# Kernel tuning notes

Hardware: AMD Instinct MI355X
Metric: run time of the kernel (lower is better)

The kernel has to match this reference:

```python
import jax, jax.numpy as jnp
import numpy as np

B, M, T, H = 256, 80, 1000, 128


def setup_inputs() -> dict:
    key = jax.random.key(0)
    k1, k2, k3, k4, k5 = jax.random.split(key, 5)
    s = 1.0 / np.sqrt(H)
    x = jax.random.normal(k1, (B, M, T), dtype=jnp.float32)
    W_ih = jax.random.uniform(k2, (3 * H, M), dtype=jnp.float32, minval=-s, maxval=s)
    W_hh = jax.random.uniform(k3, (3 * H, H), dtype=jnp.float32, minval=-s, maxval=s)
    b_ih = jax.random.uniform(k4, (3 * H,), dtype=jnp.float32, minval=-s, maxval=s)
    b_hh = jax.random.uniform(k5, (3 * H,), dtype=jnp.float32, minval=-s, maxval=s)
    return {"x": x, "W_ih": W_ih, "W_hh": W_hh, "b_ih": b_ih, "b_hh": b_hh}


def reference(x, W_ih, W_hh, b_ih, b_hh):
    # x: (B, n_mels, T) -> (B, T, n_mels)
    xt = jnp.swapaxes(x, 1, 2)
    # Precompute input-side gate projections for all timesteps: (B, T, 3H)
    gx_all = jnp.einsum('btm,gm->btg', xt, W_ih) + b_ih
    gx_seq = jnp.swapaxes(gx_all, 0, 1)  # (T, B, 3H)

    def step(h, gx):
        gh = h @ W_hh.T + b_hh  # (B, 3H)
        xr, xz, xn = jnp.split(gx, 3, axis=-1)
        hr, hz, hn = jnp.split(gh, 3, axis=-1)
        r = jax.nn.sigmoid(xr + hr)
        z = jax.nn.sigmoid(xz + hz)
        n = jnp.tanh(xn + r * hn)
        h_new = (1.0 - z) * n + z * h
        return h_new, None

    h0 = jnp.zeros((x.shape[0], H), dtype=x.dtype)
    hT, _ = jax.lax.scan(step, h0, gx_seq)
    return hT  # (B, H) == hidden[-1]
```

## Files before the change

kernel.cpp:

```cpp
#include <hip/hip_runtime.h>
#include <stdint.h>

#define B_   256
#define M_   80
#define T_   1000
#define H_   128
#define TILE 32
#define NT_  32
#define XPAD 104
#define GXS  520

typedef _Float16 half8  __attribute__((ext_vector_type(8)));
typedef _Float16 half4v __attribute__((ext_vector_type(4)));
typedef float    f32x4  __attribute__((ext_vector_type(4)));

#define LOG2E 1.44269504f
#define MFMA(A, Bf, C) __builtin_amdgcn_mfma_f32_16x16x32_f16((A), (Bf), (C), 0, 0, 0)

__device__ __forceinline__ float fast_sigmoid(float v) {
    return __builtin_amdgcn_rcpf(1.0f + __builtin_amdgcn_exp2f(-LOG2E * v));
}
__device__ __forceinline__ float fast_tanh(float v) {
    return fmaf(-2.0f, __builtin_amdgcn_rcpf(1.0f + __builtin_amdgcn_exp2f(2.0f * LOG2E * v)), 1.0f);
}

__global__ __launch_bounds__(512, 2) void gru_tile(
    const float* __restrict__ x,
    const float* __restrict__ W_ih,
    const float* __restrict__ W_hh,
    const float* __restrict__ b_ih,
    const float* __restrict__ b_hh,
    float* __restrict__ out)
{
    const int b   = blockIdx.x;
    const int tid = threadIdx.x;
    const int l   = tid & 63;
    const int w   = tid >> 6;
    const int jn  = l & 15;
    const int kq  = l >> 4;
    const int hid = 16 * w + jn;

    __shared__ __align__(16) _Float16 gxt[TILE][GXS];
    __shared__ __align__(16) _Float16 xt16[2][TILE][XPAD];
    __shared__ __align__(16) _Float16 h16[2][H_];

    half8 wr[4], wz[4], wn[4];
#pragma unroll
    for (int f = 0; f < 4; ++f)
#pragma unroll
        for (int j = 0; j < 8; ++j) {
            const int k = 32 * f + 8 * kq + j;
            wr[f][j] = (_Float16)W_hh[(hid)          * H_ + k];
            wz[f][j] = (_Float16)W_hh[(H_ + hid)     * H_ + k];
            wn[f][j] = (_Float16)W_hh[(2 * H_ + hid) * H_ + k];
        }
#pragma unroll
    for (int f = 0; f < 4; ++f) {
        asm volatile("" : "+v"(wr[f]));
        asm volatile("" : "+v"(wz[f]));
        asm volatile("" : "+v"(wn[f]));
    }

    half8 wih[3][3];
    float biasA[3];
#pragma unroll
    for (int i = 0; i < 3; ++i) {
        const int g = 16 * (3 * w + i) + jn;
        biasA[i] = b_ih[g] + (g < 2 * H_ ? b_hh[g] : 0.0f);
        const float* wp = W_ih + g * M_;
#pragma unroll
        for (int f = 0; f < 3; ++f)
#pragma unroll
            for (int j = 0; j < 8; ++j) {
                const int k = 32 * f + 8 * kq + j;
                wih[i][f][j] = (k < M_) ? (_Float16)wp[k] : (_Float16)0.0f;
            }
    }
#pragma unroll
    for (int i = 0; i < 3; ++i) {
        asm volatile("" : "+v"(wih[i][0]));
        asm volatile("" : "+v"(wih[i][1]));
        asm volatile("" : "+v"(wih[i][2]));
    }
    asm volatile("" : "+v"(biasA[0]), "+v"(biasA[1]), "+v"(biasA[2]));

    const float bN = b_hh[2 * H_ + hid];
    const f32x4 zero4 = { 0.f, 0.f, 0.f, 0.f };
    const f32x4 bN4   = { bN, bN, bN, bN };
    const float* xb = x + (size_t)b * M_ * T_;

    for (int i = tid; i < 2 * TILE * XPAD; i += 512) ((short*)xt16)[i] = 0;
    if (tid < H_) h16[0][tid] = (_Float16)0.0f;
    __syncthreads();
    {
        const int tq = tid & 7, m0 = tid >> 3;
        float4 v0 = *(const float4*)&xb[(size_t)m0 * T_ + 4 * tq];
#pragma unroll
        for (int e = 0; e < 4; ++e) xt16[0][4 * tq + e][m0] = (_Float16)v0[e];
        if (tid < 128) {
            float4 v1 = *(const float4*)&xb[(size_t)(64 + m0) * T_ + 4 * tq];
#pragma unroll
            for (int e = 0; e < 4; ++e) xt16[0][4 * tq + e][64 + m0] = (_Float16)v1[e];
        }
    }
    __syncthreads();

    float h_r = 0.0f;

#define GRU_STEP(RB, WB, CA, PA_, TN)                                         \
    {                                                                         \
        const int ko = 8 * kq;                                                \
        const half8 a0 = *(const half8*)&h16[RB][ko];                         \
        const half8 a2 = *(const half8*)&h16[RB][64 + ko];                    \
        const half8 a1 = *(const half8*)&h16[RB][32 + ko];                    \
        const half8 a3 = *(const half8*)&h16[RB][96 + ko];                    \
        PA_ = *(const half4v*)&gxt[TN][hid * 4];                              \
        const float gr = (float)CA[0], gz = (float)CA[1], gn = (float)CA[2];  \
        f32x4 Ra = MFMA(a0, wr[0], zero4);                                    \
        f32x4 Na = MFMA(a0, wn[0], bN4);                                      \
        f32x4 Rb = MFMA(a2, wr[2], zero4);                                    \
        f32x4 Nb = MFMA(a2, wn[2], zero4);                                    \
        Ra = MFMA(a1, wr[1], Ra);                                             \
        Na = MFMA(a1, wn[1], Na);                                             \
        Rb = MFMA(a3, wr[3], Rb);                                             \
        Nb = MFMA(a3, wn[3], Nb);                                             \
        f32x4 Zc = MFMA(a0, wz[0], zero4);                                    \
        Zc = MFMA(a1, wz[1], Zc);                                             \
        Zc = MFMA(a2, wz[2], Zc);                                             \
        Zc = MFMA(a3, wz[3], Zc);                                             \
        const float r  = fast_sigmoid(Ra[0] + Rb[0] + gr);                    \
        const float nv = fast_tanh(fmaf(r, Na[0] + Nb[0], gn));               \
        const float z  = fast_sigmoid(Zc[0] + gz);                            \
        h_r = fmaf(z, h_r - nv, nv);                                          \
        if (l < 16) h16[WB][hid] = (_Float16)h_r;                             \
    }

    for (int tb = 0; tb < NT_; ++tb) {
        const int t1 = TILE * (tb + 1);
        const int tq = tid & 7, m0 = tid >> 3;
        float4 xv0, xv1;
        const bool doPref = (t1 < T_);
        if (doPref) {
            const int tc0 = t1 + 4 * tq;
            const int tc  = (tc0 <= T_ - 4) ? tc0 : (T_ - 4);
            xv0 = *(const float4*)&xb[(size_t)m0 * T_ + tc];
            if (tid < 128) xv1 = *(const float4*)&xb[(size_t)(64 + m0) * T_ + tc];
        }
        const int cbuf = tb & 1, nbuf = cbuf ^ 1;
#pragma unroll
        for (int mt = 0; mt < 2; ++mt) {
            half8 af[3];
#pragma unroll
            for (int f = 0; f < 3; ++f)
                af[f] = *(const half8*)&xt16[cbuf][16 * mt + jn][32 * f + 8 * kq];
#pragma unroll
            for (int i = 0; i < 3; ++i) {
                f32x4 acc = { biasA[i], biasA[i], biasA[i], biasA[i] };
                acc = MFMA(af[0], wih[i][0], acc);
                acc = MFMA(af[1], wih[i][1], acc);
                acc = MFMA(af[2], wih[i][2], acc);
                const int g    = 16 * (3 * w + i) + jn;
                const int cc   = (g & 127) * 4 + (g >> 7);
                const int trow = 16 * mt + 4 * kq;
#pragma unroll
                for (int r2 = 0; r2 < 4; ++r2)
                    gxt[trow + r2][cc] = (_Float16)acc[r2];
            }
        }
        if (doPref) {
#pragma unroll
            for (int e = 0; e < 4; ++e) xt16[nbuf][4 * tq + e][m0] = (_Float16)xv0[e];
            if (tid < 128) {
#pragma unroll
                for (int e = 0; e < 4; ++e) xt16[nbuf][4 * tq + e][64 + m0] = (_Float16)xv1[e];
            }
        }
        __syncthreads();

        const int rem    = T_ - TILE * tb;
        const int nsteps = (rem < TILE) ? rem : TILE;

        half4v gC = *(const half4v*)&gxt[0][hid * 4];
        half4v gP;

        for (int tt = 0; tt < nsteps; tt += 2) {
            GRU_STEP(0, 1, gC, gP, tt + 1);
            __syncthreads();
            const int tn2 = (tt + 2 < nsteps) ? (tt + 2) : 0;
            GRU_STEP(1, 0, gP, gC, tn2);
            __syncthreads();
        }
    }

    if (l < 16) out[(size_t)b * H_ + hid] = h_r;
}

extern "C" void kernel_launch(void* const* d_in, const int* in_sizes, int n_in,
                              void* d_out, int out_size, void* d_ws, size_t ws_size,
                              hipStream_t stream) {
    const float* x    = (const float*)d_in[0];
    const float* W_ih = (const float*)d_in[1];
    const float* W_hh = (const float*)d_in[2];
    const float* b_ih = (const float*)d_in[3];
    const float* b_hh = (const float*)d_in[4];
    float* out = (float*)d_out;

    gru_tile<<<dim3(B_), dim3(512), 0, stream>>>(x, W_ih, W_hh, b_ih, b_hh, out);
}
```

Measured before the change: 459.5 us.

## Software-pipeline input projection across recurrent steps with double-buffered gate tile

The input-gate projection for the next time tile is now computed one MFMA triple at a time between recurrent steps of the current tile, instead of in a separate phase before each tile's recurrence. The gate buffer becomes double-buffered with an XOR-swizzled layout to reduce LDS bank conflicts, and the x prefetch is moved two tiles ahead. s_setprio is raised around the recurrent MFMA chain. The aim is to hide the per-tile projection and sync latency inside the serial recurrence, at the cost of more LDS and more complex indexing.

Measured after the change: 513.9 us. 1.12x slower.

```diff
diff --git a/kernel.cpp b/kernel.cpp
--- a/kernel.cpp
+++ b/kernel.cpp
@@ -22,6 +22,10 @@
 }
 __device__ __forceinline__ float fast_tanh(float v) {
     return fmaf(-2.0f, __builtin_amdgcn_rcpf(1.0f + __builtin_amdgcn_exp2f(2.0f * LOG2E * v)), 1.0f);
+}
+
+__device__ __forceinline__ int gx_off(int t, int hp, int i) {
+    return t * (GXS * 2) + ((((hp) << 3) + ((i) << 1)) ^ ((((t) >> 2) & 7) << 4));
 }
 
 __global__ __launch_bounds__(512, 2) void gru_tile(
@@ -40,7 +44,7 @@
     const int kq  = l >> 4;
     const int hid = 16 * w + jn;
 
-    __shared__ __align__(16) _Float16 gxt[TILE][GXS];
+    __shared__ __align__(16) _Float16 gxt[2][TILE][GXS];
     __shared__ __align__(16) _Float16 xt16[2][TILE][XPAD];
     __shared__ __align__(16) _Float16 h16[2][H_];
 
@@ -65,8 +69,8 @@
     float biasA[3];
 #pragma unroll
     for (int i = 0; i < 3; ++i) {
-        const int g = 16 * (3 * w + i) + jn;
-        biasA[i] = b_ih[g] + (g < 2 * H_ ? b_hh[g] : 0.0f);
+        const int g = 128 * i + hid;
+        biasA[i] = b_ih[g] + (i < 2 ? b_hh[g] : 0.0f);
         const float* wp = W_ih + g * M_;
 #pragma unroll
         for (int f = 0; f < 3; ++f)
@@ -88,12 +92,12 @@
     const f32x4 zero4 = { 0.f, 0.f, 0.f, 0.f };
     const f32x4 bN4   = { bN, bN, bN, bN };
     const float* xb = x + (size_t)b * M_ * T_;
+    const int tq = tid & 7, m0 = tid >> 3;
 
     for (int i = tid; i < 2 * TILE * XPAD; i += 512) ((short*)xt16)[i] = 0;
     if (tid < H_) h16[0][tid] = (_Float16)0.0f;
     __syncthreads();
     {
-        const int tq = tid & 7, m0 = tid >> 3;
         float4 v0 = *(const float4*)&xb[(size_t)m0 * T_ + 4 * tq];
 #pragma unroll
         for (int e = 0; e < 4; ++e) xt16[0][4 * tq + e][m0] = (_Float16)v0[e];
@@ -101,6 +105,43 @@
             float4 v1 = *(const float4*)&xb[(size_t)(64 + m0) * T_ + 4 * tq];
 #pragma unroll
             for (int e = 0; e < 4; ++e) xt16[0][4 * tq + e][64 + m0] = (_Float16)v1[e];
+        }
+    }
+    __syncthreads();
+
+#define PHASEA_TRIPLE(MT, I, XS, GD)                                          \
+    {                                                                         \
+        const half8 af0 = *(const half8*)&(XS)[16 * (MT) + jn][8 * kq];       \
+        const half8 af1 = *(const half8*)&(XS)[16 * (MT) + jn][32 + 8 * kq];  \
+        const half8 af2 = *(const half8*)&(XS)[16 * (MT) + jn][64 + 8 * kq];  \
+        f32x4 acc = { biasA[I], biasA[I], biasA[I], biasA[I] };               \
+        acc = MFMA(af0, wih[I][0], acc);                                      \
+        acc = MFMA(af1, wih[I][1], acc);                                      \
+        acc = MFMA(af2, wih[I][2], acc);                                      \
+        const int trow = 16 * (MT) + 4 * kq;                                  \
+        *(_Float16*)((GD) + gx_off(trow + 0, hid, (I))) = (_Float16)acc[0];   \
+        *(_Float16*)((GD) + gx_off(trow + 1, hid, (I))) = (_Float16)acc[1];   \
+        *(_Float16*)((GD) + gx_off(trow + 2, hid, (I))) = (_Float16)acc[2];   \
+        *(_Float16*)((GD) + gx_off(trow + 3, hid, (I))) = (_Float16)acc[3];   \
+    }
+
+    {
+        float4 xv0 = *(const float4*)&xb[(size_t)m0 * T_ + TILE + 4 * tq];
+        float4 xv1;
+        if (tid < 128) xv1 = *(const float4*)&xb[(size_t)(64 + m0) * T_ + TILE + 4 * tq];
+        const _Float16 (*xS0)[XPAD] = xt16[0];
+        char* g0 = (char*)&gxt[0][0][0];
+        PHASEA_TRIPLE(0, 0, xS0, g0);
+        PHASEA_TRIPLE(0, 1, xS0, g0);
+        PHASEA_TRIPLE(0, 2, xS0, g0);
+        PHASEA_TRIPLE(1, 0, xS0, g0);
+        PHASEA_TRIPLE(1, 1, xS0, g0);
+        PHASEA_TRIPLE(1, 2, xS0, g0);
+#pragma unroll
+        for (int e = 0; e < 4; ++e) xt16[1][4 * tq + e][m0] = (_Float16)xv0[e];
+        if (tid < 128) {
+#pragma unroll
+            for (int e = 0; e < 4; ++e) xt16[1][4 * tq + e][64 + m0] = (_Float16)xv1[e];
         }
     }
     __syncthreads();
@@ -114,8 +155,9 @@
         const half8 a2 = *(const half8*)&h16[RB][64 + ko];                    \
         const half8 a1 = *(const half8*)&h16[RB][32 + ko];                    \
         const half8 a3 = *(const half8*)&h16[RB][96 + ko];                    \
-        PA_ = *(const half4v*)&gxt[TN][hid * 4];                              \
+        PA_ = *(const half4v*)(gcur + gx_off((TN), hid, 0));                  \
         const float gr = (float)CA[0], gz = (float)CA[1], gn = (float)CA[2];  \
+        __builtin_amdgcn_s_setprio(1);                                        \
         f32x4 Ra = MFMA(a0, wr[0], zero4);                                    \
         f32x4 Na = MFMA(a0, wn[0], bN4);                                      \
         f32x4 Rb = MFMA(a2, wr[2], zero4);                                    \
@@ -128,6 +170,7 @@
         Zc = MFMA(a1, wz[1], Zc);                                             \
         Zc = MFMA(a2, wz[2], Zc);                                             \
         Zc = MFMA(a3, wz[3], Zc);                                             \
+        __builtin_amdgcn_s_setprio(0);                                        \
         const float r  = fast_sigmoid(Ra[0] + Rb[0] + gr);                    \
         const float nv = fast_tanh(fmaf(r, Na[0] + Nb[0], gn));               \
         const float z  = fast_sigmoid(Zc[0] + gz);                            \
@@ -136,57 +179,49 @@
     }
 
     for (int tb = 0; tb < NT_; ++tb) {
-        const int t1 = TILE * (tb + 1);
-        const int tq = tid & 7, m0 = tid >> 3;
+        const int cg = tb & 1, ng = cg ^ 1;
+        const char* gcur = (const char*)&gxt[cg][0][0];
+        char*       gnxt = (char*)&gxt[ng][0][0];
+        const _Float16 (*xS)[XPAD] = xt16[ng];
+        const bool mkNext = (tb + 1 < NT_);
+        const bool pfX    = (tb + 2 < NT_);
+        const int rem   = T_ - TILE * tb;
+        const int niter = ((rem < TILE) ? rem : TILE) >> 1;
+
         float4 xv0, xv1;
-        const bool doPref = (t1 < T_);
-        if (doPref) {
-            const int tc0 = t1 + 4 * tq;
-            const int tc  = (tc0 <= T_ - 4) ? tc0 : (T_ - 4);
-            xv0 = *(const float4*)&xb[(size_t)m0 * T_ + tc];
-            if (tid < 128) xv1 = *(const float4*)&xb[(size_t)(64 + m0) * T_ + tc];
-        }
-        const int cbuf = tb & 1, nbuf = cbuf ^ 1;
-#pragma unroll
-        for (int mt = 0; mt < 2; ++mt) {
-            half8 af[3];
-#pragma unroll
-            for (int f = 0; f < 3; ++f)
-                af[f] = *(const half8*)&xt16[cbuf][16 * mt + jn][32 * f + 8 * kq];
-#pragma unroll
-            for (int i = 0; i < 3; ++i) {
-                f32x4 acc = { biasA[i], biasA[i], biasA[i], biasA[i] };
-                acc = MFMA(af[0], wih[i][0], acc);
-                acc = MFMA(af[1], wih[i][1], acc);
-                acc = MFMA(af[2], wih[i][2], acc);
-                const int g    = 16 * (3 * w + i) + jn;
-                const int cc   = (g & 127) * 4 + (g >> 7);
-                const int trow = 16 * mt + 4 * kq;
-#pragma unroll
-                for (int r2 = 0; r2 < 4; ++r2)
-                    gxt[trow + r2][cc] = (_Float16)acc[r2];
+        half4v gC = *(const half4v*)(gcur + gx_off(0, hid, 0));
+        half4v gP;
+
+        for (int it = 0; it < niter; ++it) {
+            const int tt = 2 * it;
+            GRU_STEP(0, 1, gC, gP, tt + 1);
+            if (pfX && it == 0) {
+                const int tc0 = TILE * (tb + 2) + 4 * tq;
+                const int tc  = (tc0 <= T_ - 4) ? tc0 : (T_ - 4);
+                xv0 = *(const float4*)&xb[(size_t)m0 * T_ + tc];
+                if (tid < 128) xv1 = *(const float4*)&xb[(size_t)(64 + m0) * T_ + tc];
             }
-        }
-        if (doPref) {
-#pragma unroll
-            for (int e = 0; e < 4; ++e) xt16[nbuf][4 * tq + e][m0] = (_Float16)xv0[e];
-            if (tid < 128) {
-#pragma unroll
-                for (int e = 0; e < 4; ++e) xt16[nbuf][4 * tq + e][64 + m0] = (_Float16)xv1[e];
+            __syncthreads();
+            if (mkNext) {
+                switch (it) {
+                    case 0: PHASEA_TRIPLE(0, 0, xS, gnxt); break;
+                    case 1: PHASEA_TRIPLE(0, 1, xS, gnxt); break;
+                    case 2: PHASEA_TRIPLE(0, 2, xS, gnxt); break;
+                    case 3: PHASEA_TRIPLE(1, 0, xS, gnxt); break;
+                    case 4: PHASEA_TRIPLE(1, 1, xS, gnxt); break;
+                    case 5: PHASEA_TRIPLE(1, 2, xS, gnxt); break;
+                    default: break;
+                }
+                if (pfX && it == 6) {
+#pragma unroll
+                    for (int e = 0; e < 4; ++e) xt16[cg][4 * tq + e][m0] = (_Float16)xv0[e];
+                    if (tid < 128) {
+#pragma unroll
+                        for (int e = 0; e < 4; ++e) xt16[cg][4 * tq + e][64 + m0] = (_Float16)xv1[e];
+                    }
+                }
             }
-        }
-        __syncthreads();
-
-        const int rem    = T_ - TILE * tb;
-        const int nsteps = (rem < TILE) ? rem : TILE;
-
-        half4v gC = *(const half4v*)&gxt[0][hid * 4];
-        half4v gP;
-
-        for (int tt = 0; tt < nsteps; tt += 2) {
-            GRU_STEP(0, 1, gC, gP, tt + 1);
-            __syncthreads();
-            const int tn2 = (tt + 2 < nsteps) ? (tt + 2) : 0;
+            const int tn2 = (tt + 2 < 2 * niter) ? (tt + 2) : 0;
             GRU_STEP(1, 0, gP, gC, tn2);
             __syncthreads();
         }
```
